# Optimization experiments

Hardware: AMD Instinct MI355X
Metric: run time of the kernel (lower is better)

## Reference

```python
import jax, jax.numpy as jnp
import numpy as np

TOT_LEN, MEM_LEN, BSZ = 1024, 1024, 4
SEG_LEN = TOT_LEN + MEM_LEN
D_EMBED, N_HEAD, D_HEAD = 1024, 16, 64


def setup_inputs() -> dict:
    key = jax.random.key(0)
    ks = jax.random.split(key, 8)
    sc = 0.02
    w = jax.random.normal(ks[0], (TOT_LEN, BSZ, D_EMBED), jnp.float32)
    r = jax.random.normal(ks[1], (SEG_LEN, D_EMBED), jnp.float32)
    r_w_bias = jax.random.normal(ks[2], (N_HEAD, D_HEAD), jnp.float32) * sc
    r_r_bias = jax.random.normal(ks[3], (N_HEAD, D_HEAD), jnp.float32) * sc
    mems = jax.random.normal(ks[4], (MEM_LEN, BSZ, D_EMBED), jnp.float32)
    Wqkv = jax.random.normal(ks[5], (D_EMBED, 3 * N_HEAD * D_HEAD), jnp.float32) * sc
    Wr = jax.random.normal(ks[6], (D_EMBED, N_HEAD * D_HEAD), jnp.float32) * sc
    Wo = jax.random.normal(ks[7], (N_HEAD * D_HEAD, D_EMBED), jnp.float32) * sc
    # causal mask: query i may attend to keys j <= i + MEM_LEN; True = disallow
    i = jnp.arange(TOT_LEN)[:, None]
    j = jnp.arange(SEG_LEN)[None, :]
    attn_mask = (j > i + MEM_LEN)[:, :, None]  # (tot_len, seg_len, 1) bool
    return {"w": w, "r": r, "r_w_bias": r_w_bias, "r_r_bias": r_r_bias,
            "attn_mask": attn_mask, "mems": mems, "Wqkv": Wqkv, "Wr": Wr, "Wo": Wo}


def _rel_shift(x):
    # x: (i, j, b, n) -> Transformer-XL relative shift
    i, j, b, n = x.shape
    x = jnp.pad(x, ((0, 0), (1, 0), (0, 0), (0, 0)))  # zero-pad along j
    x = x.reshape(j + 1, i, b, n)[1:].reshape(i, j, b, n)
    return x


def reference(w, r, r_w_bias, r_r_bias, attn_mask, mems, Wqkv, Wr, Wo):
    tot_len, bsz, _ = w.shape
    seg_len = r.shape[0]
    scale = 1.0 / (D_HEAD ** 0.5)
    cat = jnp.concatenate([mems, w], axis=0)            # (S, b, E)
    w_heads = cat @ Wqkv                                 # (S, b, 3*H*D)
    q, k, v = jnp.split(w_heads, 3, axis=-1)
    q = q[-tot_len:].reshape(tot_len, bsz, N_HEAD, D_HEAD)
    k = k.reshape(seg_len, bsz, N_HEAD, D_HEAD)
    v = v.reshape(seg_len, bsz, N_HEAD, D_HEAD)
    r_head_k = (r @ Wr).reshape(seg_len, N_HEAD, D_HEAD)
    AC = jnp.einsum('ibnd,jbnd->ijbn', q + r_w_bias, k)
    BD = jnp.einsum('ibnd,jnd->ijbn', q + r_r_bias, r_head_k)
    BD = _rel_shift(BD)
    attn_score = (AC + BD) * scale                       # (i, j, b, n)
    attn_score = jnp.where(attn_mask[:, :, :, None], -jnp.inf, attn_score)
    attn_prob = jax.nn.softmax(attn_score, axis=1)
    attn_vec = jnp.einsum('ijbn,jbnd->ibnd', attn_prob, v)
    attn_vec = attn_vec.reshape(tot_len, bsz, N_HEAD * D_HEAD)
    return attn_vec @ Wo
```

## Files before the change

### kernel.cpp

```cpp
#include <hip/hip_runtime.h>
#include <cstddef>


static constexpr int kTot = 1024;
static constexpr int kMem = 1024;
static constexpr int kSeg = 2048;
static constexpr int kBsz = 4;
static constexpr int kEmb = 1024;
static constexpr int kNH  = 16;
static constexpr int kDH  = 64;

typedef __attribute__((ext_vector_type(8))) short bf16x8;
typedef __attribute__((ext_vector_type(4))) float f32x4;
typedef unsigned short ushort_t;

__device__ __forceinline__ ushort_t f2bf(float f) {
    union { float f; unsigned u; } v; v.f = f;
    unsigned r = v.u + 0x7fffu + ((v.u >> 16) & 1u);
    return (ushort_t)(r >> 16);
}

__device__ __forceinline__ void gl_lds16(const ushort_t* g, ushort_t* l) {
    __builtin_amdgcn_global_load_lds(
        (const __attribute__((address_space(1))) unsigned int*)g,
        (__attribute__((address_space(3))) unsigned int*)l, 16, 0, 0);
}

__global__ __launch_bounds__(256) void cvt3_kernel(
    const float* __restrict__ mems, const float* __restrict__ w,
    const float* __restrict__ r,
    ushort_t* __restrict__ cat_bf, ushort_t* __restrict__ r_a)
{
    const int i = blockIdx.x * 256 + threadIdx.x;
    const float* src;
    ushort_t* dst;
    if (i < 524288)        { src = mems + (size_t)i * 8;             dst = cat_bf + (size_t)i * 8; }
    else if (i < 1048576)  { src = w + (size_t)(i - 524288) * 8;     dst = cat_bf + (size_t)i * 8; }
    else                   { src = r + (size_t)(i - 1048576) * 8;    dst = r_a + (size_t)(i - 1048576) * 8; }
    const float4 a = ((const float4*)src)[0];
    const float4 b = ((const float4*)src)[1];
    ushort_t o[8] = {f2bf(a.x), f2bf(a.y), f2bf(a.z), f2bf(a.w),
                     f2bf(b.x), f2bf(b.y), f2bf(b.z), f2bf(b.w)};
    *(uint4*)dst = *(const uint4*)o;
}

__global__ __launch_bounds__(256) void transpose3_kernel(
    const float* __restrict__ Wqkv, const float* __restrict__ Wr,
    const float* __restrict__ Wo,
    ushort_t* __restrict__ wqkvT, ushort_t* __restrict__ wrT,
    ushort_t* __restrict__ woT)
{
    __shared__ ushort_t Ts[64][72];
    const int bid = blockIdx.x;
    const float* src; ushort_t* dst; int N, rel;
    if (bid < 768)       { src = Wqkv; dst = wqkvT; N = 3072; rel = bid; }
    else if (bid < 1024) { src = Wr;   dst = wrT;   N = 1024; rel = bid - 768; }
    else                 { src = Wo;   dst = woT;   N = 1024; rel = bid - 1024; }
    const int nx = N >> 6;
    const int n0 = (rel % nx) << 6;
    const int k0 = (rel / nx) << 6;
    const int t  = threadIdx.x;
#pragma unroll
    for (int g2 = 0; g2 < 4; ++g2) {
        const int kl  = (t >> 4) + g2 * 16;
        const int nl4 = (t & 15) * 4;
        const float4 v = *(const float4*)(src + (size_t)(k0 + kl) * N + n0 + nl4);
        Ts[nl4 + 0][kl] = f2bf(v.x);
        Ts[nl4 + 1][kl] = f2bf(v.y);
        Ts[nl4 + 2][kl] = f2bf(v.z);
        Ts[nl4 + 3][kl] = f2bf(v.w);
    }
    __syncthreads();
    const int nl = t >> 2;
    const int c  = (t & 3) * 16;
    ushort_t tmp[16];
#pragma unroll
    for (int e = 0; e < 16; ++e) tmp[e] = Ts[nl][c + e];
    ushort_t* drow = dst + (size_t)(n0 + nl) * 1024 + k0 + c;
    *(uint4*)drow       = *(const uint4*)tmp;
    *(uint4*)(drow + 8) = *(const uint4*)(tmp + 8);
}

template<int MODE>
__global__ __launch_bounds__(256) void gemm_bf16_kernel(
    const ushort_t* __restrict__ A, const ushort_t* __restrict__ B,
    float* __restrict__ outq, ushort_t* __restrict__ outk, ushort_t* __restrict__ outv)
{
    __shared__ ushort_t Al[128 * 64];
    __shared__ ushort_t Bl[128 * 64];

    const int t    = threadIdx.x;
    const int lane = t & 63;
    const int w    = t >> 6;
    const int c15  = lane & 15;
    const int g    = lane >> 4;
    const int wr   = w >> 1;
    const int wc   = w & 1;
    const int n0   = blockIdx.x * 128;
    const int m0   = blockIdx.y * 128;

    const int srow = t >> 3;
    const int scc  = t & 7;
    const int wbase = (t & ~63);

    const f32x4 z4 = {0.f, 0.f, 0.f, 0.f};
    f32x4 acc[4][4];
#pragma unroll
    for (int mb = 0; mb < 4; ++mb)
#pragma unroll
        for (int nb = 0; nb < 4; ++nb) acc[mb][nb] = z4;

    for (int k0 = 0; k0 < kEmb; k0 += 64) {
        __syncthreads();
        const ushort_t* Ab = A + (size_t)m0 * kEmb + k0;
        const ushort_t* Bb = B + (size_t)n0 * kEmb + k0;
#pragma unroll
        for (int q = 0; q < 4; ++q) {
            const int row  = q * 32 + srow;
            const int gcol = scc ^ (row & 7);
            gl_lds16(Ab + (size_t)row * kEmb + gcol * 8, Al + (q * 256 + wbase) * 8);
            gl_lds16(Bb + (size_t)row * kEmb + gcol * 8, Bl + (q * 256 + wbase) * 8);
        }
        __syncthreads();
#pragma unroll
        for (int ks = 0; ks < 2; ++ks) {
            bf16x8 af[4], bfr[4];
#pragma unroll
            for (int mb = 0; mb < 4; ++mb) {
                const int row = wr * 64 + mb * 16 + c15;
                af[mb] = *(const bf16x8*)((const char*)Al + row * 128 +
                           ((ks * 64 + g * 16) ^ ((row & 7) << 4)));
            }
#pragma unroll
            for (int nb = 0; nb < 4; ++nb) {
                const int row = wc * 64 + nb * 16 + c15;
                bfr[nb] = *(const bf16x8*)((const char*)Bl + row * 128 +
                            ((ks * 64 + g * 16) ^ ((row & 7) << 4)));
            }
#pragma unroll
            for (int mb = 0; mb < 4; ++mb)
#pragma unroll
                for (int nb = 0; nb < 4; ++nb)
                    acc[mb][nb] = __builtin_amdgcn_mfma_f32_16x16x32_bf16(
                        af[mb], bfr[nb], acc[mb][nb], 0, 0, 0);
        }
    }

#pragma unroll
    for (int mb = 0; mb < 4; ++mb) {
#pragma unroll
        for (int ri = 0; ri < 4; ++ri) {
            const int gm = m0 + wr * 64 + mb * 16 + g * 4 + ri;
#pragma unroll
            for (int nb = 0; nb < 4; ++nb) {
                const int gn    = n0 + wc * 64 + nb * 16 + c15;
                const float val = acc[mb][nb][ri];
                if (MODE == 0) {
                    const int s = gm >> 2, b = gm & 3;
                    const int part = gn >> 10, within = gn & 1023;
                    const int hn = within >> 6, d = within & 63;
                    if (part == 0) {
                        if (s >= kMem)
                            outq[(((size_t)(b * kNH + hn) * kTot + (s - kMem)) << 6) + d] = val;
                    } else if (part == 1) {
                        outk[(((size_t)(b * kNH + hn) * kSeg + s) << 6) + d] = f2bf(val);
                    } else {
                        outv[(((size_t)(b * kNH + hn) * kSeg + s) << 6) + d] = f2bf(val);
                    }
                } else if (MODE == 1) {
                    const int hn = gn >> 6, d = gn & 63;
                    outk[(((size_t)hn * kSeg + gm) << 6) + d] = f2bf(val);
                } else {
                    outq[(size_t)gm * 1024 + gn] = val;
                }
            }
        }
    }
}

__global__ __launch_bounds__(256, 4) void attn_kernel(
    const float* __restrict__ q_ws, const ushort_t* __restrict__ k_bf,
    const ushort_t* __restrict__ v_bf, const ushort_t* __restrict__ r_bf,
    const float* __restrict__ rwb, const float* __restrict__ rrb,
    ushort_t* __restrict__ av_bf)
{
    __shared__ char lds[40960];
    char* Kl = lds;
    char* Rl = lds + 8192;
    char* Vl = lds + 24576;
    char* Pl = lds + 32768;

    const int t    = threadIdx.x;
    const int lane = t & 63;
    const int w    = t >> 6;
    const int c15  = lane & 15;
    const int g    = lane >> 4;
    const int swz  = (c15 & 7) << 4;

    const int xr   = blockIdx.x;
    const int iblk = (xr & 1) ? (15 - (xr >> 1)) : (xr >> 1);
    const int i0   = iblk << 6;
    const int h    = blockIdx.y;
    const int b    = h >> 4, n = h & 15;
    const int iw0  = i0 + w * 16;

    const float*    qbase = q_ws + ((size_t)h * kTot << 6);
    const ushort_t* kbase = k_bf + ((size_t)h * kSeg << 6);
    const ushort_t* vbase = v_bf + ((size_t)h * kSeg << 6);
    const ushort_t* rbase = r_bf + ((size_t)n * kSeg << 6);

    bf16x8 qw[2], qr[2];
    {
        const float* qrow = qbase + ((size_t)(iw0 + c15) << 6);
        const float* wb = rwb + n * 64;
        const float* rb = rrb + n * 64;
#pragma unroll
        for (int ks = 0; ks < 2; ++ks) {
            const int d0 = ks * 32 + g * 8;
#pragma unroll
            for (int e = 0; e < 8; ++e) {
                const float qv = qrow[d0 + e];
                qw[ks][e] = (short)f2bf(qv + wb[d0 + e]);
                qr[ks][e] = (short)f2bf(qv + rb[d0 + e]);
            }
        }
    }

    const int jrowK = t >> 2, dqK = t & 3;
    const int jv = t & 63,  dqv = t >> 6;
    const int qR = t >> 2,  cR  = t & 3;

    {
        const ushort_t* src = kbase + ((size_t)jrowK << 6) + dqK * 16;
        const uint4 a0 = ((const uint4*)src)[0];
        const uint4 a1 = ((const uint4*)src)[1];
        const int rs = (jrowK & 7) << 4;
        const int colA = dqK << 5;
        *(uint4*)(Kl + (jrowK << 7) + (colA ^ rs))        = a0;
        *(uint4*)(Kl + (jrowK << 7) + ((colA + 16) ^ rs)) = a1;
    }
    {
        const int row = t >> 1, hf = t & 1;
        const int rel = 960 - i0 + row;
        const ushort_t* src = rbase + ((size_t)rel << 6) + hf * 32;
        const uint4 rv0 = ((const uint4*)src)[0];
        const uint4 rv1 = ((const uint4*)src)[1];
        const uint4 rv2 = ((const uint4*)src)[2];
        const uint4 rv3 = ((const uint4*)src)[3];
        const int rs = (row & 7) << 4;
        char* base = Rl + (row << 7);
        const int cb2 = hf << 6;
        *(uint4*)(base + ((cb2 +  0) ^ rs)) = rv0;
        *(uint4*)(base + ((cb2 + 16) ^ rs)) = rv1;
        *(uint4*)(base + ((cb2 + 32) ^ rs)) = rv2;
        *(uint4*)(base + ((cb2 + 48) ^ rs)) = rv3;
    }
    {
        const ushort_t* src = vbase + ((size_t)jv << 6) + dqv * 16;
        ushort_t tmp[16];
        *(uint4*)tmp       = ((const uint4*)src)[0];
        *(uint4*)(tmp + 8) = ((const uint4*)src)[1];
#pragma unroll
        for (int e = 0; e < 16; ++e) {
            const int d = dqv * 16 + e;
            *(ushort_t*)(Vl + (d << 7) + ((jv << 1) ^ ((d & 7) << 4))) = tmp[e];
        }
    }

    const f32x4 z4 = {0.f, 0.f, 0.f, 0.f};
    f32x4 o[4] = {z4, z4, z4, z4};
    float m_run[4] = {-1e30f, -1e30f, -1e30f, -1e30f};
    float l_run[4] = {0.f, 0.f, 0.f, 0.f};

    const int ntiles = (i0 + 1151) >> 6;
    for (int tile = 0; tile < ntiles; ++tile) {
        const int j0   = tile << 6;
        const int rxor = (tile & 1) << 6;

        __syncthreads();

        const bool pf = (tile + 1 < ntiles);
        uint4 kr0, kr1, vr0, vr1, rr0, rr1;
        if (pf) {
            const uint4 z = {0u, 0u, 0u, 0u};
            kr0 = kr1 = vr0 = vr1 = rr0 = rr1 = z;
            const int j1 = j0 + 64;
            const int jK = j1 + jrowK;
            if (jK < kSeg) {
                const ushort_t* src = kbase + ((size_t)jK << 6) + dqK * 16;
                kr0 = ((const uint4*)src)[0];
                kr1 = ((const uint4*)src)[1];
            }
            const int jV = j1 + jv;
            if (jV < kSeg) {
                const ushort_t* src = vbase + ((size_t)jV << 6) + dqv * 16;
                vr0 = ((const uint4*)src)[0];
                vr1 = ((const uint4*)src)[1];
            }
            const int relN = j1 - i0 + 1024 + qR;
            if (relN < kSeg) {
                const ushort_t* src = rbase + ((size_t)relN << 6) + cR * 16;
                rr0 = ((const uint4*)src)[0];
                rr1 = ((const uint4*)src)[1];
            }
        }

        f32x4 ac[4] = {z4, z4, z4, z4};
#pragma unroll
        for (int nb = 0; nb < 4; ++nb) {
#pragma unroll
            for (int ks = 0; ks < 2; ++ks) {
                const int row = nb * 16 + c15;
                const bf16x8 kf = *(const bf16x8*)(Kl + (row << 7) +
                                   (((ks << 6) | (g << 4)) ^ swz));
                ac[nb] = __builtin_amdgcn_mfma_f32_16x16x32_bf16(qw[ks], kf, ac[nb], 0, 0, 0);
            }
        }
        f32x4 bd[5] = {z4, z4, z4, z4, z4};
        const int rw0 = 48 - 16 * w;
#pragma unroll
        for (int cb = 0; cb < 5; ++cb) {
#pragma unroll
            for (int ks = 0; ks < 2; ++ks) {
                const int lr = rw0 + cb * 16 + c15;
                const int pr = lr ^ rxor;
                const bf16x8 rf = *(const bf16x8*)(Rl + (pr << 7) +
                                   (((ks << 6) | (g << 4)) ^ swz));
                bd[cb] = __builtin_amdgcn_mfma_f32_16x16x32_bf16(qr[ks], rf, bd[cb], 0, 0, 0);
            }
        }

        float s[4][4];
#pragma unroll
        for (int r = 0; r < 4; ++r) {
            const int sh   = 15 - 4 * g - r;
            const int idx  = c15 + sh;
            const int srcl = (lane & 48) | (idx & 15);
            float shv[5];
#pragma unroll
            for (int cb = 0; cb < 5; ++cb) shv[cb] = __shfl(bd[cb][r], srcl);
            const int irow = iw0 + 4 * g + r;
#pragma unroll
            for (int nb = 0; nb < 4; ++nb) {
                const float bdv = (idx >= 16) ? shv[nb + 1] : shv[nb];
                const float sv  = (ac[nb][r] + bdv) * 0.125f;
                const int j     = j0 + nb * 16 + c15;
                s[nb][r] = (j <= irow + kMem) ? sv : -1e30f;
            }
        }

        const int pbase = (w << 11);
#pragma unroll
        for (int r = 0; r < 4; ++r) {
            float mt = fmaxf(fmaxf(s[0][r], s[1][r]), fmaxf(s[2][r], s[3][r]));
            mt = fmaxf(mt, __shfl_xor(mt, 1));
            mt = fmaxf(mt, __shfl_xor(mt, 2));
            mt = fmaxf(mt, __shfl_xor(mt, 4));
            mt = fmaxf(mt, __shfl_xor(mt, 8));
            const float mnew = fmaxf(m_run[r], mt);
            const float al   = __expf(m_run[r] - mnew);
            float p[4];
#pragma unroll
            for (int nb = 0; nb < 4; ++nb) p[nb] = __expf(s[nb][r] - mnew);
            l_run[r] = l_run[r] * al + (p[0] + p[1]) + (p[2] + p[3]);
            m_run[r] = mnew;
            const int il  = 4 * g + r;
            const int isw = (il & 7) << 4;
#pragma unroll
            for (int nb = 0; nb < 4; ++nb) {
                o[nb][r] *= al;
                *(ushort_t*)(Pl + pbase + (il << 7) +
                             (((nb << 5) + (c15 << 1)) ^ isw)) = f2bf(p[nb]);
            }
        }

        bf16x8 pfr[2];
#pragma unroll
        for (int ks = 0; ks < 2; ++ks)
            pfr[ks] = *(const bf16x8*)(Pl + pbase + (c15 << 7) +
                        (((ks << 6) | (g << 4)) ^ swz));
#pragma unroll
        for (int nb = 0; nb < 4; ++nb) {
#pragma unroll
            for (int ks = 0; ks < 2; ++ks) {
                const int row = nb * 16 + c15;
                const bf16x8 vf = *(const bf16x8*)(Vl + (row << 7) +
                                   (((ks << 6) | (g << 4)) ^ swz));
                o[nb] = __builtin_amdgcn_mfma_f32_16x16x32_bf16(pfr[ks], vf, o[nb], 0, 0, 0);
            }
        }

        __syncthreads();

        if (pf) {
            {
                const int rs = (jrowK & 7) << 4;
                const int colA = dqK << 5;
                *(uint4*)(Kl + (jrowK << 7) + (colA ^ rs))        = kr0;
                *(uint4*)(Kl + (jrowK << 7) + ((colA + 16) ^ rs)) = kr1;
            }
            {
                const int pr = qR ^ rxor;
                const int rs = (qR & 7) << 4;
                const int colR = cR << 5;
                *(uint4*)(Rl + (pr << 7) + (colR ^ rs))        = rr0;
                *(uint4*)(Rl + (pr << 7) + ((colR + 16) ^ rs)) = rr1;
            }
            {
                ushort_t tmp[16];
                *(uint4*)tmp       = vr0;
                *(uint4*)(tmp + 8) = vr1;
#pragma unroll
                for (int e = 0; e < 16; ++e) {
                    const int d = dqv * 16 + e;
                    *(ushort_t*)(Vl + (d << 7) + ((jv << 1) ^ ((d & 7) << 4))) = tmp[e];
                }
            }
        }
    }

#pragma unroll
    for (int r = 0; r < 4; ++r) {
        float lsum = l_run[r];
        lsum += __shfl_xor(lsum, 1);
        lsum += __shfl_xor(lsum, 2);
        lsum += __shfl_xor(lsum, 4);
        lsum += __shfl_xor(lsum, 8);
        const float inv = 1.0f / lsum;
        const int irow  = iw0 + 4 * g + r;
#pragma unroll
        for (int nb = 0; nb < 4; ++nb) {
            av_bf[(((size_t)(irow * 4 + b)) << 10) + n * 64 + nb * 16 + c15] =
                f2bf(o[nb][r] * inv);
        }
    }
}


extern "C" void kernel_launch(void* const* d_in, const int* in_sizes, int n_in,
                              void* d_out, int out_size, void* d_ws, size_t ws_size,
                              hipStream_t stream) {
    (void)in_sizes; (void)n_in; (void)out_size; (void)ws_size;

    const float* w    = (const float*)d_in[0];
    const float* r    = (const float*)d_in[1];
    const float* rwb  = (const float*)d_in[2];
    const float* rrb  = (const float*)d_in[3];
    const float* mems = (const float*)d_in[5];
    const float* Wqkv = (const float*)d_in[6];
    const float* Wr   = (const float*)d_in[7];
    const float* Wo   = (const float*)d_in[8];
    float* out = (float*)d_out;

    char* ws = (char*)d_ws;
    ushort_t* cat_bf = (ushort_t*)ws;
    ushort_t* wqkvT  = (ushort_t*)(ws + (16u << 20));
    ushort_t* wrT    = (ushort_t*)(ws + (22u << 20));
    ushort_t* r_a    = (ushort_t*)(ws + (24u << 20));
    float*    q_ws   = (float*)   (ws + (28u << 20));
    ushort_t* k_bf   = (ushort_t*)(ws + (44u << 20));
    ushort_t* v_bf   = (ushort_t*)(ws + (60u << 20));
    ushort_t* r_bf   = (ushort_t*)(ws + (76u << 20));
    ushort_t* av_bf  = (ushort_t*)(ws + (80u << 20));
    ushort_t* woT    = (ushort_t*)(ws + (88u << 20));

    cvt3_kernel<<<5120, 256, 0, stream>>>(mems, w, r, cat_bf, r_a);
    transpose3_kernel<<<1280, 256, 0, stream>>>(Wqkv, Wr, Wo, wqkvT, wrT, woT);

    gemm_bf16_kernel<0><<<dim3(24, 64), 256, 0, stream>>>(cat_bf, wqkvT, q_ws, k_bf, v_bf);
    gemm_bf16_kernel<1><<<dim3(8, 16), 256, 0, stream>>>(r_a, wrT, nullptr, r_bf, nullptr);

    attn_kernel<<<dim3(16, 64), 256, 0, stream>>>(q_ws, k_bf, v_bf, r_bf, rwb, rrb, av_bf);

    gemm_bf16_kernel<2><<<dim3(8, 32), 256, 0, stream>>>(av_bf, woT, out, nullptr, nullptr);
}
```

Baseline: 583.9 us.

## Read K/R/V fragments directly from global memory per wave, drop LDS staging

The attention kernel no longer stages K, R and V tiles in shared memory with block-wide barriers. Each wave now loads its MFMA fragments straight from global memory, and V is written pre-transposed (d-major) by the QKV GEMM so those loads are contiguous. Waves are assigned balanced causal strips (pairing short and long rows), the block index is remapped so heads sharing r are co-scheduled for cache reuse, and the 1/sqrt(d) scale is folded into q. This removes the syncthreads and LDS traffic, but relies on L1/L2 to absorb the redundant per-wave global reads, and the uncoalesced transposed V store in the GEMM epilogue may cost extra.

```diff
diff --git a/kernel.cpp b/kernel.cpp
--- a/kernel.cpp
+++ b/kernel.cpp
@@ -165,7 +165,7 @@
                     } else if (part == 1) {
                         outk[(((size_t)(b * kNH + hn) * kSeg + s) << 6) + d] = f2bf(val);
                     } else {
-                        outv[(((size_t)(b * kNH + hn) * kSeg + s) << 6) + d] = f2bf(val);
+                        outv[((size_t)(b * kNH + hn) * kDH + d) * kSeg + s] = f2bf(val);
                     }
                 } else if (MODE == 1) {
                     const int hn = gn >> 6, d = gn & 63;
@@ -178,17 +178,13 @@
     }
 }
 
-__global__ __launch_bounds__(256, 4) void attn_kernel(
+__global__ __launch_bounds__(256) void attn_kernel(
     const float* __restrict__ q_ws, const ushort_t* __restrict__ k_bf,
-    const ushort_t* __restrict__ v_bf, const ushort_t* __restrict__ r_bf,
+    const ushort_t* __restrict__ v_t, const ushort_t* __restrict__ r_bf,
     const float* __restrict__ rwb, const float* __restrict__ rrb,
     ushort_t* __restrict__ av_bf)
 {
-    __shared__ char lds[40960];
-    char* Kl = lds;
-    char* Rl = lds + 8192;
-    char* Vl = lds + 24576;
-    char* Pl = lds + 32768;
+    __shared__ char Pl_all[8192];
 
     const int t    = threadIdx.x;
     const int lane = t & 63;
@@ -197,17 +193,24 @@
     const int g    = lane >> 4;
     const int swz  = (c15 & 7) << 4;
 
-    const int xr   = blockIdx.x;
-    const int iblk = (xr & 1) ? (15 - (xr >> 1)) : (xr >> 1);
-    const int i0   = iblk << 6;
-    const int h    = blockIdx.y;
-    const int b    = h >> 4, n = h & 15;
-    const int iw0  = i0 + w * 16;
-
-    const float*    qbase = q_ws + ((size_t)h * kTot << 6);
-    const ushort_t* kbase = k_bf + ((size_t)h * kSeg << 6);
-    const ushort_t* vbase = v_bf + ((size_t)h * kSeg << 6);
-    const ushort_t* rbase = r_bf + ((size_t)n * kSeg << 6);
+    const int bid = blockIdx.x;
+    const int xc  = bid & 7;
+    const int kk  = bid >> 3;
+    const int jb  = kk & 15;
+    const int n   = xc + ((kk >> 4) & 1) * 8;
+    const int b   = kk >> 5;
+    const int h   = b * 16 + n;
+
+    const int strip = (w == 0) ? (2 * jb)
+                    : (w == 1) ? (2 * jb + 1)
+                    : (w == 2) ? (62 - 2 * jb)
+                               : (63 - 2 * jb);
+    const int iw0 = strip << 4;
+
+    const float*    qbase = q_ws + ((size_t)h << 16);
+    const ushort_t* kbase = k_bf + ((size_t)h << 17);
+    const ushort_t* vbase = v_t  + ((size_t)h << 17);
+    const ushort_t* rbase = r_bf + ((size_t)n << 17);
 
     bf16x8 qw[2], qr[2];
     {
@@ -220,112 +223,45 @@
 #pragma unroll
             for (int e = 0; e < 8; ++e) {
                 const float qv = qrow[d0 + e];
-                qw[ks][e] = (short)f2bf(qv + wb[d0 + e]);
-                qr[ks][e] = (short)f2bf(qv + rb[d0 + e]);
-            }
-        }
-    }
-
-    const int jrowK = t >> 2, dqK = t & 3;
-    const int jv = t & 63,  dqv = t >> 6;
-    const int qR = t >> 2,  cR  = t & 3;
-
-    {
-        const ushort_t* src = kbase + ((size_t)jrowK << 6) + dqK * 16;
-        const uint4 a0 = ((const uint4*)src)[0];
-        const uint4 a1 = ((const uint4*)src)[1];
-        const int rs = (jrowK & 7) << 4;
-        const int colA = dqK << 5;
-        *(uint4*)(Kl + (jrowK << 7) + (colA ^ rs))        = a0;
-        *(uint4*)(Kl + (jrowK << 7) + ((colA + 16) ^ rs)) = a1;
-    }
-    {
-        const int row = t >> 1, hf = t & 1;
-        const int rel = 960 - i0 + row;
-        const ushort_t* src = rbase + ((size_t)rel << 6) + hf * 32;
-        const uint4 rv0 = ((const uint4*)src)[0];
-        const uint4 rv1 = ((const uint4*)src)[1];
-        const uint4 rv2 = ((const uint4*)src)[2];
-        const uint4 rv3 = ((const uint4*)src)[3];
-        const int rs = (row & 7) << 4;
-        char* base = Rl + (row << 7);
-        const int cb2 = hf << 6;
-        *(uint4*)(base + ((cb2 +  0) ^ rs)) = rv0;
-        *(uint4*)(base + ((cb2 + 16) ^ rs)) = rv1;
-        *(uint4*)(base + ((cb2 + 32) ^ rs)) = rv2;
-        *(uint4*)(base + ((cb2 + 48) ^ rs)) = rv3;
-    }
-    {
-        const ushort_t* src = vbase + ((size_t)jv << 6) + dqv * 16;
-        ushort_t tmp[16];
-        *(uint4*)tmp       = ((const uint4*)src)[0];
-        *(uint4*)(tmp + 8) = ((const uint4*)src)[1];
-#pragma unroll
-        for (int e = 0; e < 16; ++e) {
-            const int d = dqv * 16 + e;
-            *(ushort_t*)(Vl + (d << 7) + ((jv << 1) ^ ((d & 7) << 4))) = tmp[e];
-        }
-    }
+                qw[ks][e] = (short)f2bf((qv + wb[d0 + e]) * 0.125f);
+                qr[ks][e] = (short)f2bf((qv + rb[d0 + e]) * 0.125f);
+            }
+        }
+    }
+
+    char* Pl = Pl_all + (w << 11);
 
     const f32x4 z4 = {0.f, 0.f, 0.f, 0.f};
     f32x4 o[4] = {z4, z4, z4, z4};
     float m_run[4] = {-1e30f, -1e30f, -1e30f, -1e30f};
     float l_run[4] = {0.f, 0.f, 0.f, 0.f};
 
-    const int ntiles = (i0 + 1151) >> 6;
+    const int ntiles = (iw0 + 1103) >> 6;
     for (int tile = 0; tile < ntiles; ++tile) {
-        const int j0   = tile << 6;
-        const int rxor = (tile & 1) << 6;
-
-        __syncthreads();
-
-        const bool pf = (tile + 1 < ntiles);
-        uint4 kr0, kr1, vr0, vr1, rr0, rr1;
-        if (pf) {
-            const uint4 z = {0u, 0u, 0u, 0u};
-            kr0 = kr1 = vr0 = vr1 = rr0 = rr1 = z;
-            const int j1 = j0 + 64;
-            const int jK = j1 + jrowK;
-            if (jK < kSeg) {
-                const ushort_t* src = kbase + ((size_t)jK << 6) + dqK * 16;
-                kr0 = ((const uint4*)src)[0];
-                kr1 = ((const uint4*)src)[1];
-            }
-            const int jV = j1 + jv;
-            if (jV < kSeg) {
-                const ushort_t* src = vbase + ((size_t)jV << 6) + dqv * 16;
-                vr0 = ((const uint4*)src)[0];
-                vr1 = ((const uint4*)src)[1];
-            }
-            const int relN = j1 - i0 + 1024 + qR;
-            if (relN < kSeg) {
-                const ushort_t* src = rbase + ((size_t)relN << 6) + cR * 16;
-                rr0 = ((const uint4*)src)[0];
-                rr1 = ((const uint4*)src)[1];
-            }
-        }
+        const int j0 = tile << 6;
 
         f32x4 ac[4] = {z4, z4, z4, z4};
 #pragma unroll
         for (int nb = 0; nb < 4; ++nb) {
+            const size_t jrow = (size_t)(j0 + nb * 16 + c15) << 6;
 #pragma unroll
             for (int ks = 0; ks < 2; ++ks) {
-                const int row = nb * 16 + c15;
-                const bf16x8 kf = *(const bf16x8*)(Kl + (row << 7) +
-                                   (((ks << 6) | (g << 4)) ^ swz));
+                const bf16x8 kf = *(const bf16x8*)(kbase + jrow + ks * 32 + g * 8);
                 ac[nb] = __builtin_amdgcn_mfma_f32_16x16x32_bf16(qw[ks], kf, ac[nb], 0, 0, 0);
             }
         }
+
         f32x4 bd[5] = {z4, z4, z4, z4, z4};
-        const int rw0 = 48 - 16 * w;
+        const int relb = j0 - iw0 + 1008;
 #pragma unroll
         for (int cb = 0; cb < 5; ++cb) {
+            const int rel = relb + cb * 16 + c15;
+            const bool rv = (rel < kSeg);
+            const size_t rrow = (size_t)rel << 6;
 #pragma unroll
             for (int ks = 0; ks < 2; ++ks) {
-                const int lr = rw0 + cb * 16 + c15;
-                const int pr = lr ^ rxor;
-                const bf16x8 rf = *(const bf16x8*)(Rl + (pr << 7) +
-                                   (((ks << 6) | (g << 4)) ^ swz));
+                bf16x8 rf = {0, 0, 0, 0, 0, 0, 0, 0};
+                if (rv) rf = *(const bf16x8*)(rbase + rrow + ks * 32 + g * 8);
                 bd[cb] = __builtin_amdgcn_mfma_f32_16x16x32_bf16(qr[ks], rf, bd[cb], 0, 0, 0);
             }
         }
@@ -343,13 +279,12 @@
 #pragma unroll
             for (int nb = 0; nb < 4; ++nb) {
                 const float bdv = (idx >= 16) ? shv[nb + 1] : shv[nb];
-                const float sv  = (ac[nb][r] + bdv) * 0.125f;
+                const float sv  = ac[nb][r] + bdv;
                 const int j     = j0 + nb * 16 + c15;
                 s[nb][r] = (j <= irow + kMem) ? sv : -1e30f;
             }
         }
 
-        const int pbase = (w << 11);
 #pragma unroll
         for (int r = 0; r < 4; ++r) {
             float mt = fmaxf(fmaxf(s[0][r], s[1][r]), fmaxf(s[2][r], s[3][r]));
@@ -369,7 +304,7 @@
 #pragma unroll
             for (int nb = 0; nb < 4; ++nb) {
                 o[nb][r] *= al;
-                *(ushort_t*)(Pl + pbase + (il << 7) +
+                *(ushort_t*)(Pl + (il << 7) +
                              (((nb << 5) + (c15 << 1)) ^ isw)) = f2bf(p[nb]);
             }
         }
@@ -377,44 +312,15 @@
         bf16x8 pfr[2];
 #pragma unroll
         for (int ks = 0; ks < 2; ++ks)
-            pfr[ks] = *(const bf16x8*)(Pl + pbase + (c15 << 7) +
+            pfr[ks] = *(const bf16x8*)(Pl + (c15 << 7) +
                         (((ks << 6) | (g << 4)) ^ swz));
 #pragma unroll
         for (int nb = 0; nb < 4; ++nb) {
+            const size_t drow = (size_t)(nb * 16 + c15) << 11;
 #pragma unroll
             for (int ks = 0; ks < 2; ++ks) {
-                const int row = nb * 16 + c15;
-                const bf16x8 vf = *(const bf16x8*)(Vl + (row << 7) +
-                                   (((ks << 6) | (g << 4)) ^ swz));
+                const bf16x8 vf = *(const bf16x8*)(vbase + drow + j0 + ks * 32 + g * 8);
                 o[nb] = __builtin_amdgcn_mfma_f32_16x16x32_bf16(pfr[ks], vf, o[nb], 0, 0, 0);
-            }
-        }
-
-        __syncthreads();
-
-        if (pf) {
-            {
-                const int rs = (jrowK & 7) << 4;
-                const int colA = dqK << 5;
-                *(uint4*)(Kl + (jrowK << 7) + (colA ^ rs))        = kr0;
-                *(uint4*)(Kl + (jrowK << 7) + ((colA + 16) ^ rs)) = kr1;
-            }
-            {
-                const int pr = qR ^ rxor;
-                const int rs = (qR & 7) << 4;
-                const int colR = cR << 5;
-                *(uint4*)(Rl + (pr << 7) + (colR ^ rs))        = rr0;
-                *(uint4*)(Rl + (pr << 7) + ((colR + 16) ^ rs)) = rr1;
-            }
-            {
-                ushort_t tmp[16];
-                *(uint4*)tmp       = vr0;
-                *(uint4*)(tmp + 8) = vr1;
-#pragma unroll
-                for (int e = 0; e < 16; ++e) {
-                    const int d = dqv * 16 + e;
-                    *(ushort_t*)(Vl + (d << 7) + ((jv << 1) ^ ((d & 7) << 4))) = tmp[e];
-                }
             }
         }
     }
@@ -459,7 +365,7 @@
     ushort_t* r_a    = (ushort_t*)(ws + (24u << 20));
     float*    q_ws   = (float*)   (ws + (28u << 20));
     ushort_t* k_bf   = (ushort_t*)(ws + (44u << 20));
-    ushort_t* v_bf   = (ushort_t*)(ws + (60u << 20));
+    ushort_t* v_t    = (ushort_t*)(ws + (60u << 20));
     ushort_t* r_bf   = (ushort_t*)(ws + (76u << 20));
     ushort_t* av_bf  = (ushort_t*)(ws + (80u << 20));
     ushort_t* woT    = (ushort_t*)(ws + (88u << 20));
@@ -467,10 +373,10 @@
     cvt3_kernel<<<5120, 256, 0, stream>>>(mems, w, r, cat_bf, r_a);
     transpose3_kernel<<<1280, 256, 0, stream>>>(Wqkv, Wr, Wo, wqkvT, wrT, woT);
 
-    gemm_bf16_kernel<0><<<dim3(24, 64), 256, 0, stream>>>(cat_bf, wqkvT, q_ws, k_bf, v_bf);
+    gemm_bf16_kernel<0><<<dim3(24, 64), 256, 0, stream>>>(cat_bf, wqkvT, q_ws, k_bf, v_t);
     gemm_bf16_kernel<1><<<dim3(8, 16), 256, 0, stream>>>(r_a, wrT, nullptr, r_bf, nullptr);
 
-    attn_kernel<<<dim3(16, 64), 256, 0, stream>>>(q_ws, k_bf, v_bf, r_bf, rwb, rrb, av_bf);
+    attn_kernel<<<1024, 256, 0, stream>>>(q_ws, k_bf, v_t, r_bf, rwb, rrb, av_bf);
 
     gemm_bf16_kernel<2><<<dim3(8, 32), 256, 0, stream>>>(av_bf, woT, out, nullptr, nullptr);
 }
```

After: 680.0 us. 1.16x slower.
